# Kernel tuning notes

Hardware: AMD Instinct MI355X
Metric: run time of the kernel (lower is better)

The kernel has to match this reference:

```python
import jax, jax.numpy as jnp
import numpy as np

B, S, H = 2, 2048, 4096
NH, NKV, HD = 32, 8, 128
THETA = 1000000.0
NEG = jnp.finfo(jnp.float32).min


def setup_inputs() -> dict:
    key = jax.random.key(0)
    ks = jax.random.split(key, 9)
    s = 0.02
    return {
        "hidden_states": jax.random.normal(ks[0], (B, S, H), jnp.float32),
        "position_ids": jnp.tile(jnp.arange(S, dtype=jnp.int32)[None, :], (B, 1)),
        "Wq": jax.random.normal(ks[1], (NH * HD, H), jnp.float32) * s,
        "bq": jax.random.normal(ks[2], (NH * HD,), jnp.float32) * s,
        "Wk": jax.random.normal(ks[3], (NKV * HD, H), jnp.float32) * s,
        "bk": jax.random.normal(ks[4], (NKV * HD,), jnp.float32) * s,
        "Wv": jax.random.normal(ks[5], (NKV * HD, H), jnp.float32) * s,
        "bv": jax.random.normal(ks[6], (NKV * HD,), jnp.float32) * s,
        "Wo": jax.random.normal(ks[7], (H, H), jnp.float32) * s,
        "bo": jax.random.normal(ks[8], (H,), jnp.float32) * s,
    }


def _rotate_half_interleaved(x):
    # y[..., ::2] = -x[..., 1::2]; y[..., 1::2] = x[..., ::2]
    x2 = x.reshape(*x.shape[:-1], -1, 2)
    y = jnp.stack([-x2[..., 1], x2[..., 0]], axis=-1)
    return y.reshape(x.shape)


def reference(hidden_states, position_ids, Wq, bq, Wk, bk, Wv, bv, Wo, bo):
    bsz, q_len, _ = hidden_states.shape
    q = (hidden_states @ Wq.T + bq).reshape(bsz, q_len, NH, HD).transpose(0, 2, 1, 3)
    k = (hidden_states @ Wk.T + bk).reshape(bsz, q_len, NKV, HD).transpose(0, 2, 1, 3)
    v = (hidden_states @ Wv.T + bv).reshape(bsz, q_len, NKV, HD).transpose(0, 2, 1, 3)

    # rotary embedding (interleaved / repeat_interleave variant)
    inv_freq = 1.0 / (THETA ** (jnp.arange(0, HD, 2, dtype=jnp.float32) / HD))
    freqs = position_ids.astype(jnp.float32)[:, :, None] * inv_freq[None, None, :]  # [B,S,HD/2]
    emb = jnp.repeat(freqs, 2, axis=-1)  # [B,S,HD]
    cos = jnp.cos(emb)[:, None, :, :]  # [B,1,S,HD]
    sin = jnp.sin(emb)[:, None, :, :]
    q = q * cos + _rotate_half_interleaved(q) * sin
    k = k * cos + _rotate_half_interleaved(k) * sin

    # GQA: repeat KV heads (repeat_interleave on head axis)
    n_rep = NH // NKV
    k = jnp.repeat(k, n_rep, axis=1)
    v = jnp.repeat(v, n_rep, axis=1)

    scores = jnp.einsum("bhqd,bhkd->bhqk", q, k) / np.sqrt(HD).astype(np.float32)
    causal = jnp.tril(jnp.ones((q_len, q_len), dtype=bool))
    scores = jnp.where(causal[None, None, :, :], scores, NEG)
    attn = jax.nn.softmax(scores.astype(jnp.float32), axis=-1).astype(q.dtype)
    out = jnp.einsum("bhqk,bhkd->bhqd", attn, v)
    out = out.transpose(0, 2, 1, 3).reshape(bsz, q_len, H)
    return out @ Wo.T + bo
```

## Files before the change

kernel.cpp:

```cpp
#include <hip/hip_runtime.h>
#include <stdint.h>

typedef __bf16 bf16x8 __attribute__((ext_vector_type(8)));
typedef float f32x4 __attribute__((ext_vector_type(4)));
typedef float f32x16 __attribute__((ext_vector_type(16)));

#define S_LEN 2048
#define NKVH 8
#define HDIM 128
#define MROWS 4096
#define LDQKV 6144
#define SCALE 0.08838834764831845f
#define C_LOG2 0.1275405707067851f
#define THR_RAW 62.7f

__device__ __forceinline__ unsigned short f2bf(float f) {
  unsigned u = __float_as_uint(f);
  u += 0x7FFFu + ((u >> 16) & 1u);
  return (unsigned short)(u >> 16);
}
__device__ __forceinline__ float bf2f(unsigned short h) {
  return __uint_as_float(((unsigned)h) << 16);
}

__device__ __forceinline__ void gload16(const unsigned short* g, unsigned short* l) {
  __builtin_amdgcn_global_load_lds(
      (__attribute__((address_space(1))) void*)(g),
      (__attribute__((address_space(3))) void*)(l), 16, 0, 0);
}

__global__ void cast_f32_bf16(const float4* __restrict__ in, ushort4* __restrict__ out, int n4) {
  int i = blockIdx.x * 256 + threadIdx.x;
  const int stride = gridDim.x * 256;
  for (; i < n4; i += stride) {
    float4 v = in[i];
    ushort4 o;
    o.x = f2bf(v.x); o.y = f2bf(v.y); o.z = f2bf(v.z); o.w = f2bf(v.w);
    out[i] = o;
  }
}

template <int OUTF>
__global__ __launch_bounds__(512, 2)
void gemm256(const unsigned short* __restrict__ A,
             const unsigned short* __restrict__ Bw,
             const float* __restrict__ bias,
             void* __restrict__ C,
             int ldc, int K) {
  __shared__ unsigned short lds[2][4][8192];

  const int t = threadIdx.x;
  const int lane = t & 63;
  const int w = t >> 6;
  const int wr = w >> 2, wc = w & 3;
  const int row16 = lane & 15, kgrp = lane >> 4;
  const int m0 = blockIdx.y * 256, n0 = blockIdx.x * 256;

  const int riu = t >> 3;
  const int col = (((t & 7) ^ (riu & 7)) << 3);
  const int rB0 = (riu & 31) + ((riu >> 5) << 6);
  const unsigned short* pA = A + (size_t)(m0 + riu) * K + col;
  const unsigned short* pB = Bw + (size_t)(n0 + rB0) * K + col;

#define STG(nb_, u_, src_)                                                  \
  {                                                                         \
    gload16((src_), &lds[nb_][u_][t * 8]);                                  \
    gload16((src_) + (size_t)128 * K, &lds[nb_][u_][4096 + t * 8]);         \
  }

  const int sw = row16 & 7;
  const int abase = (wr * 64 + row16) * 64;
  const int bbase = (wc * 32 + row16) * 64;

  f32x4 acc[8][4];
#pragma unroll
  for (int i = 0; i < 8; i++)
#pragma unroll
    for (int j = 0; j < 4; j++) acc[i][j] = (f32x4){0.f, 0.f, 0.f, 0.f};

  bf16x8 afr[4][2], bfr[2][2][2];
  const int NT = K >> 6;

  STG(0, 0, pA);
  STG(0, 1, pB);
  STG(0, 2, pB + (size_t)32 * K);
  STG(0, 3, pA + (size_t)64 * K);

  for (int T = 0; T < NT; ++T) {
    const int cb = T & 1, nb = cb ^ 1;
    const unsigned short* Lc = &lds[cb][0][0];
    const size_t kk = (size_t)(T + 1) << 6;
    const bool st = (T + 1 < NT);

    asm volatile("s_waitcnt vmcnt(4)\n\ts_barrier" ::: "memory");
    if (st) STG(nb, 0, pA + kk);
#pragma unroll
    for (int mi = 0; mi < 4; mi++)
#pragma unroll
      for (int ks = 0; ks < 2; ks++)
        afr[mi][ks] = *(const bf16x8*)(Lc + abase + mi * 1024 + ((((ks << 2) + kgrp) ^ sw) << 3));
#pragma unroll
    for (int nj = 0; nj < 2; nj++)
#pragma unroll
      for (int ks = 0; ks < 2; ks++)
        bfr[0][nj][ks] = *(const bf16x8*)(Lc + 8192 + bbase + nj * 1024 + ((((ks << 2) + kgrp) ^ sw) << 3));
    __builtin_amdgcn_s_setprio(1);
#pragma unroll
    for (int mi = 0; mi < 4; mi++)
#pragma unroll
      for (int nj = 0; nj < 2; nj++)
#pragma unroll
        for (int ks = 0; ks < 2; ks++)
          acc[mi][nj] = __builtin_amdgcn_mfma_f32_16x16x32_bf16(afr[mi][ks], bfr[0][nj][ks], acc[mi][nj], 0, 0, 0);
    __builtin_amdgcn_s_setprio(0);

    if (st) {
      asm volatile("s_waitcnt vmcnt(4)\n\ts_barrier" ::: "memory");
      STG(nb, 1, pB + kk);
    } else {
      asm volatile("s_waitcnt vmcnt(2)\n\ts_barrier" ::: "memory");
    }
#pragma unroll
    for (int nj = 0; nj < 2; nj++)
#pragma unroll
      for (int ks = 0; ks < 2; ks++)
        bfr[1][nj][ks] = *(const bf16x8*)(Lc + 16384 + bbase + nj * 1024 + ((((ks << 2) + kgrp) ^ sw) << 3));
    __builtin_amdgcn_s_setprio(1);
#pragma unroll
    for (int mi = 0; mi < 4; mi++)
#pragma unroll
      for (int nj = 0; nj < 2; nj++)
#pragma unroll
        for (int ks = 0; ks < 2; ks++)
          acc[mi][2 + nj] = __builtin_amdgcn_mfma_f32_16x16x32_bf16(afr[mi][ks], bfr[1][nj][ks], acc[mi][2 + nj], 0, 0, 0);
    __builtin_amdgcn_s_setprio(0);

    if (st) {
      asm volatile("s_waitcnt vmcnt(4)\n\ts_barrier" ::: "memory");
      STG(nb, 2, pB + (size_t)32 * K + kk);
    } else {
      asm volatile("s_waitcnt vmcnt(0)\n\ts_barrier" ::: "memory");
    }
#pragma unroll
    for (int mi = 0; mi < 4; mi++)
#pragma unroll
      for (int ks = 0; ks < 2; ks++)
        afr[mi][ks] = *(const bf16x8*)(Lc + 24576 + abase + mi * 1024 + ((((ks << 2) + kgrp) ^ sw) << 3));
    __builtin_amdgcn_s_setprio(1);
#pragma unroll
    for (int mi = 0; mi < 4; mi++)
#pragma unroll
      for (int nj = 0; nj < 2; nj++)
#pragma unroll
        for (int ks = 0; ks < 2; ks++)
          acc[4 + mi][2 + nj] = __builtin_amdgcn_mfma_f32_16x16x32_bf16(afr[mi][ks], bfr[1][nj][ks], acc[4 + mi][2 + nj], 0, 0, 0);
    __builtin_amdgcn_s_setprio(0);

    if (st) {
      asm volatile("s_waitcnt vmcnt(4)\n\ts_barrier" ::: "memory");
      STG(nb, 3, pA + (size_t)64 * K + kk);
    } else {
      asm volatile("s_barrier" ::: "memory");
    }
    __builtin_amdgcn_s_setprio(1);
#pragma unroll
    for (int mi = 0; mi < 4; mi++)
#pragma unroll
      for (int nj = 0; nj < 2; nj++)
#pragma unroll
        for (int ks = 0; ks < 2; ks++)
          acc[4 + mi][nj] = __builtin_amdgcn_mfma_f32_16x16x32_bf16(afr[mi][ks], bfr[0][nj][ks], acc[4 + mi][nj], 0, 0, 0);
    __builtin_amdgcn_s_setprio(0);
  }
#undef STG

#pragma unroll
  for (int MI = 0; MI < 8; MI++) {
#pragma unroll
    for (int NJ = 0; NJ < 4; NJ++) {
      const int gr = m0 + wr * 128 + MI * 16 + kgrp * 4;
      const int gc = n0 + wc * 64 + NJ * 16 + row16;
      const float bv = bias[gc];
#pragma unroll
      for (int jj = 0; jj < 4; jj++) {
        float v = acc[MI][NJ][jj] + bv;
        if (OUTF) ((float*)C)[(size_t)(gr + jj) * ldc + gc] = v;
        else ((unsigned short*)C)[(size_t)(gr + jj) * ldc + gc] = f2bf(v);
      }
    }
  }
}

template <int OUTF>
__global__ __launch_bounds__(512, 2)
void gemm128(const unsigned short* __restrict__ A,
             const unsigned short* __restrict__ Bw,
             const float* __restrict__ bias,
             void* __restrict__ C,
             int ldc, int K) {
  __shared__ unsigned short lds[3 * 24576];

  const int t = threadIdx.x;
  const int lane = t & 63;
  const int w = t >> 6;
  const int wr = w >> 2, wc = w & 3;
  const int row16 = lane & 15, kgrp = lane >> 4;
  const int m0 = blockIdx.y * 128, n0 = blockIdx.x * 256;

  const int riu = t >> 3;
  const int col = (((t & 7) ^ (riu & 7)) << 3);
  const unsigned short* pA = A + (size_t)(m0 + riu) * K + col;
  const unsigned short* pB = Bw + (size_t)(n0 + riu) * K + col;

#define STG6(bo_, kk_)                                                      \
  {                                                                         \
    gload16(pA + (kk_), &lds[(bo_) + t * 8]);                               \
    gload16(pA + (size_t)64 * K + (kk_), &lds[(bo_) + 4096 + t * 8]);       \
    gload16(pB + (kk_), &lds[(bo_) + 8192 + t * 8]);                        \
    gload16(pB + (size_t)64 * K + (kk_), &lds[(bo_) + 12288 + t * 8]);      \
    gload16(pB + (size_t)128 * K + (kk_), &lds[(bo_) + 16384 + t * 8]);     \
    gload16(pB + (size_t)192 * K + (kk_), &lds[(bo_) + 20480 + t * 8]);     \
  }

  const int sw = row16 & 7;
  const int abase = (wr * 64 + row16) * 64;
  const int bbase = 8192 + (wc * 64 + row16) * 64;

  f32x4 acc[4][4];
#pragma unroll
  for (int i = 0; i < 4; i++)
#pragma unroll
    for (int j = 0; j < 4; j++) acc[i][j] = (f32x4){0.f, 0.f, 0.f, 0.f};

  bf16x8 afr[4][2], bfr[4][2];
  const int NT = K >> 6;

  STG6(0, 0);
  STG6(24576, 64);

  int rbc = 0;
  int rbs = 2;
  for (int T = 0; T < NT; ++T) {
    if (T < NT - 1) { asm volatile("s_waitcnt vmcnt(6)\n\ts_barrier" ::: "memory"); }
    else            { asm volatile("s_waitcnt vmcnt(0)\n\ts_barrier" ::: "memory"); }
    if (T + 2 < NT) STG6(rbs * 24576, (size_t)(T + 2) << 6);
    const unsigned short* Lc = &lds[rbc * 24576];

#pragma unroll
    for (int mi = 0; mi < 4; mi++)
#pragma unroll
      for (int ks = 0; ks < 2; ks++)
        afr[mi][ks] = *(const bf16x8*)(Lc + abase + mi * 1024 + ((((ks << 2) + kgrp) ^ sw) << 3));
#pragma unroll
    for (int nj = 0; nj < 4; nj++)
#pragma unroll
      for (int ks = 0; ks < 2; ks++)
        bfr[nj][ks] = *(const bf16x8*)(Lc + bbase + nj * 1024 + ((((ks << 2) + kgrp) ^ sw) << 3));

    __builtin_amdgcn_s_setprio(1);
#pragma unroll
    for (int mi = 0; mi < 4; mi++)
#pragma unroll
      for (int nj = 0; nj < 4; nj++)
#pragma unroll
        for (int ks = 0; ks < 2; ks++)
          acc[mi][nj] = __builtin_amdgcn_mfma_f32_16x16x32_bf16(afr[mi][ks], bfr[nj][ks], acc[mi][nj], 0, 0, 0);
    __builtin_amdgcn_s_setprio(0);

    rbc++; if (rbc == 3) rbc = 0;
    rbs++; if (rbs == 3) rbs = 0;
  }
#undef STG6

#pragma unroll
  for (int MI = 0; MI < 4; MI++) {
#pragma unroll
    for (int NJ = 0; NJ < 4; NJ++) {
      const int gr = m0 + wr * 64 + MI * 16 + kgrp * 4;
      const int gc = n0 + wc * 64 + NJ * 16 + row16;
      const float bv = bias[gc];
#pragma unroll
      for (int jj = 0; jj < 4; jj++) {
        float v = acc[MI][NJ][jj] + bv;
        if (OUTF) ((float*)C)[(size_t)(gr + jj) * ldc + gc] = v;
        else ((unsigned short*)C)[(size_t)(gr + jj) * ldc + gc] = f2bf(v);
      }
    }
  }
}

__global__ void rope_kernel(unsigned short* __restrict__ X,
                            const int* __restrict__ pos_ids,
                            int ncols, int ld) {
  const int perrow = ncols >> 3;
  int idx = blockIdx.x * 256 + threadIdx.x;
  const int row = idx / perrow;
  const int c0 = (idx - row * perrow) << 3;
  const float pos = (float)pos_ids[row];
  unsigned short* p = X + (size_t)row * ld + c0;
  uint4 v = *(uint4*)p;
  unsigned short* e = (unsigned short*)&v;
  const int p0 = (c0 & 127) >> 1;
#pragma unroll
  for (int q = 0; q < 4; ++q) {
    const float inv = exp2f(-(float)(p0 + q) * (19.931568569324174f / 64.f));
    const float fr = pos * inv;
    float sn, cs;
    __sincosf(fr, &sn, &cs);
    const float xe = bf2f(e[2 * q]);
    const float xo = bf2f(e[2 * q + 1]);
    e[2 * q]     = f2bf(xe * cs - xo * sn);
    e[2 * q + 1] = f2bf(xo * cs + xe * sn);
  }
  *(uint4*)p = v;
}

__global__ void transpose_v(const unsigned short* __restrict__ V, int ldv,
                            unsigned short* __restrict__ Vt) {
  __shared__ unsigned short tile[32][40];
  const int t = threadIdx.x;
  const int n0 = blockIdx.x * 32;
  const int m0 = blockIdx.y * 32;
  const int r = t >> 3;
  const int c = (t & 7) << 2;
  const unsigned short* src = V + (size_t)(m0 + r) * ldv + n0 + c;
  ushort4 d = *(const ushort4*)src;
  tile[r][c] = d.x; tile[r][c + 1] = d.y; tile[r][c + 2] = d.z; tile[r][c + 3] = d.w;
  __syncthreads();
  const int b = m0 >> 11;
  unsigned short* dst = Vt + (size_t)(b * 1024 + n0 + r) * 2048 + (m0 & 2047) + c;
  ushort4 o;
  o.x = tile[c][r]; o.y = tile[c + 1][r]; o.z = tile[c + 2][r]; o.w = tile[c + 3][r];
  *(ushort4*)dst = o;
}

__global__ __launch_bounds__(256, 2)
void attn_kernel3(const unsigned short* __restrict__ QKV,
                  const unsigned short* __restrict__ Vt,
                  unsigned short* __restrict__ O) {
  __shared__ unsigned short sK[64 * 128];
  __shared__ unsigned short sV[128 * 64];

  const int t = threadIdx.x;
  const int lane = t & 63;
  const int w = t >> 6;
  const int l31 = lane & 31;
  const int hi = lane >> 5;
  const int bid = blockIdx.x;
  const int g = bid >> 6, bh = bid & 63;
  const int qt = (g < 4) ? (15 - g) : (g < 8) ? (g - 4) : (g < 12) ? (19 - g) : (g - 8);
  const int b = bh >> 5, h = bh & 31;
  const int kh = h >> 2;
  const int q0 = qt << 7;
  const int qw = q0 + w * 32;
  const int qg = qw + l31;

  const int ntiles = (q0 + 128) >> 6;
  const int myTiles = (qw + 95) >> 6;

  const int krow0 = t >> 4;
  const int kslot = t & 15;
  const int vrow0 = t >> 3;
  const int vslot = t & 7;
  const unsigned short* Kp = QKV + (size_t)(b * S_LEN) * LDQKV + 4096 + kh * HDIM;
  const unsigned short* Vp = Vt + (size_t)(b * 1024 + kh * HDIM) * 2048;
  const int ksw = (kslot ^ (krow0 & 7)) << 3;
  const int vsw = (vslot ^ (vrow0 & 7)) << 3;
  const unsigned short* KpA = Kp + (size_t)krow0 * LDQKV + ksw;
  const unsigned short* VpA = Vp + (size_t)vrow0 * 2048 + vsw;

#define STAGE(kv0m)                                                         \
  {                                                                         \
    _Pragma("unroll")                                                       \
    for (int p = 0; p < 4; p++)                                             \
      gload16(KpA + (size_t)((kv0m) + 16 * p) * LDQKV, &sK[p * 2048 + t * 8]); \
    _Pragma("unroll")                                                       \
    for (int p = 0; p < 4; p++)                                             \
      gload16(VpA + (kv0m) + p * 65536, &sV[p * 2048 + t * 8]);             \
  }

  bf16x8 qf[8];
  {
    const unsigned short* qb = QKV + (size_t)(b * S_LEN + qw + l31) * LDQKV + h * HDIM + hi * 8;
#pragma unroll
    for (int kd = 0; kd < 8; kd++) qf[kd] = *(const bf16x8*)(qb + kd * 16);
  }

  f32x16 o[4];
#pragma unroll
  for (int nt = 0; nt < 4; nt++)
#pragma unroll
    for (int r = 0; r < 16; r++) o[nt][r] = 0.f;
  float m = -1e30f, lsum = 0.f;

  const int rw7 = (l31 & 7) << 4;
  const int kswz = (hi << 4) ^ rw7;
  const int kbase0 = l31 * 128;
  const int vbase = l31 * 64;

  for (int it = 0; it < ntiles; ++it) {
    STAGE(it << 6);
    asm volatile("s_waitcnt vmcnt(0)" ::: "memory");
    __builtin_amdgcn_s_barrier();

    if (it < myTiles) {
      const int kv0 = it << 6;

      f32x16 st[2];
#pragma unroll
      for (int r = 0; r < 16; r++) { st[0][r] = 0.f; st[1][r] = 0.f; }
      __builtin_amdgcn_s_setprio(1);
#pragma unroll
      for (int kd = 0; kd < 8; kd++) {
        bf16x8 k0 = *(const bf16x8*)(sK + kbase0 + (((kd << 5) ^ kswz) >> 1));
        bf16x8 k1 = *(const bf16x8*)(sK + 4096 + kbase0 + (((kd << 5) ^ kswz) >> 1));
        st[0] = __builtin_amdgcn_mfma_f32_32x32x16_bf16(k0, qf[kd], st[0], 0, 0, 0);
        st[1] = __builtin_amdgcn_mfma_f32_32x32x16_bf16(k1, qf[kd], st[1], 0, 0, 0);
      }
      __builtin_amdgcn_s_setprio(0);

      if (it == myTiles - 1) {
#pragma unroll
        for (int s2 = 0; s2 < 2; s2++)
#pragma unroll
          for (int r = 0; r < 16; r++) {
            const int kvg = kv0 + s2 * 32 + (r & 3) + 8 * (r >> 2) + 4 * hi;
            if (kvg > qg) st[s2][r] = -1e30f;
          }
      }

      float mx[8];
#pragma unroll
      for (int r = 0; r < 8; r++)
        mx[r] = fmaxf(fmaxf(st[0][r], st[0][r + 8]), fmaxf(st[1][r], st[1][r + 8]));
#pragma unroll
      for (int d = 4; d >= 1; d >>= 1)
#pragma unroll
        for (int r = 0; r < d; r++) mx[r] = fmaxf(mx[r], mx[r + d]);
      float tmax = fmaxf(mx[0], __shfl_xor(mx[0], 32));

      if (!__all(tmax <= m + THR_RAW)) {
        const float mnew = fmaxf(m, tmax);
        const float corr = exp2f((m - mnew) * C_LOG2);
        lsum *= corr;
#pragma unroll
        for (int r = 0; r < 16; r++) {
          const int src = (r & 3) + 8 * (r >> 2) + 4 * hi;
          const float cr = __shfl(corr, src);
#pragma unroll
          for (int nt = 0; nt < 4; nt++) o[nt][r] *= cr;
        }
        m = mnew;
      }
      const float mC = m * C_LOG2;

#pragma unroll
      for (int s2 = 0; s2 < 2; s2++)
#pragma unroll
        for (int r = 0; r < 16; r++) st[s2][r] = exp2f(fmaf(st[s2][r], C_LOG2, -mC));
      float sm[8];
#pragma unroll
      for (int r = 0; r < 8; r++)
        sm[r] = (st[0][r] + st[0][r + 8]) + (st[1][r] + st[1][r + 8]);
#pragma unroll
      for (int d = 4; d >= 1; d >>= 1)
#pragma unroll
        for (int r = 0; r < d; r++) sm[r] += sm[r + d];
      float tsum = sm[0] + __shfl_xor(sm[0], 32);
      lsum += tsum;

      bf16x8 pa[4];
#pragma unroll
      for (int s2 = 0; s2 < 2; s2++) {
        unsigned pw[8];
#pragma unroll
        for (int i = 0; i < 8; i++)
          asm("v_cvt_pk_bf16_f32 %0, %1, %2" : "=v"(pw[i]) : "v"(st[s2][2 * i]), "v"(st[s2][2 * i + 1]));
        const unsigned x0 = (unsigned)__shfl_xor((int)pw[0], 32);
        const unsigned x1 = (unsigned)__shfl_xor((int)pw[1], 32);
        const unsigned x2 = (unsigned)__shfl_xor((int)pw[2], 32);
        const unsigned x3 = (unsigned)__shfl_xor((int)pw[3], 32);
        const unsigned x4 = (unsigned)__shfl_xor((int)pw[4], 32);
        const unsigned x5 = (unsigned)__shfl_xor((int)pw[5], 32);
        const unsigned x6 = (unsigned)__shfl_xor((int)pw[6], 32);
        const unsigned x7 = (unsigned)__shfl_xor((int)pw[7], 32);
        union { unsigned u[4]; bf16x8 v; } u0, u1;
        u0.u[0] = hi ? x2 : pw[0];
        u0.u[1] = hi ? x3 : pw[1];
        u0.u[2] = hi ? pw[2] : x0;
        u0.u[3] = hi ? pw[3] : x1;
        u1.u[0] = hi ? x6 : pw[4];
        u1.u[1] = hi ? x7 : pw[5];
        u1.u[2] = hi ? pw[6] : x4;
        u1.u[3] = hi ? pw[7] : x5;
        pa[2 * s2] = u0.v; pa[2 * s2 + 1] = u1.v;
      }

      __builtin_amdgcn_s_setprio(1);
#pragma unroll
      for (int nt = 0; nt < 4; nt++) {
        const unsigned short* vr = sV + vbase + nt * 2048;
#pragma unroll
        for (int ks = 0; ks < 4; ks++) {
          bf16x8 vb = *(const bf16x8*)(vr + (((ks << 5) ^ kswz) >> 1));
          o[nt] = __builtin_amdgcn_mfma_f32_32x32x16_bf16(pa[ks], vb, o[nt], 0, 0, 0);
        }
      }
      __builtin_amdgcn_s_setprio(0);
    }

    __builtin_amdgcn_s_barrier();
  }

  const float linv = 1.0f / lsum;
#pragma unroll
  for (int r = 0; r < 16; r++) {
    const int qr = (r & 3) + 8 * (r >> 2) + 4 * hi;
    const float lr = __shfl(linv, qr);
    unsigned short* orow = O + (size_t)(b * S_LEN + qw + qr) * 4096 + h * HDIM + l31;
#pragma unroll
    for (int nt = 0; nt < 4; nt++) orow[nt * 32] = f2bf(o[nt][r] * lr);
  }
#undef STAGE
}

extern "C" void kernel_launch(void* const* d_in, const int* in_sizes, int n_in,
                              void* d_out, int out_size, void* d_ws, size_t ws_size,
                              hipStream_t stream) {
  const float* hs = (const float*)d_in[0];
  const int*  pos = (const int*)d_in[1];
  const float* Wq = (const float*)d_in[2];
  const float* bq = (const float*)d_in[3];
  const float* Wk = (const float*)d_in[4];
  const float* bk = (const float*)d_in[5];
  const float* Wv = (const float*)d_in[6];
  const float* bv = (const float*)d_in[7];
  const float* Wo = (const float*)d_in[8];
  const float* bo = (const float*)d_in[9];
  float* out = (float*)d_out;

  char* ws = (char*)d_ws;
  unsigned short* hbf  = (unsigned short*)(ws);
  unsigned short* Wbuf = (unsigned short*)(ws + 33554432);
  unsigned short* QKV  = (unsigned short*)(ws + 83886080);
  unsigned short* Vtb  = (unsigned short*)(ws + 134217728);
  float*          biasb= (float*)(ws + 142606336);

  cast_f32_bf16<<<2048, 256, 0, stream>>>((const float4*)hs, (ushort4*)hbf, 4194304);
  cast_f32_bf16<<<2048, 256, 0, stream>>>((const float4*)Wq, (ushort4*)Wbuf, 4194304);
  cast_f32_bf16<<<1024, 256, 0, stream>>>((const float4*)Wk, (ushort4*)(Wbuf + 16777216), 1048576);
  cast_f32_bf16<<<1024, 256, 0, stream>>>((const float4*)Wv, (ushort4*)(Wbuf + 20971520), 1048576);
  hipMemcpyAsync(biasb, bq, 4096 * 4, hipMemcpyDeviceToDevice, stream);
  hipMemcpyAsync(biasb + 4096, bk, 1024 * 4, hipMemcpyDeviceToDevice, stream);
  hipMemcpyAsync(biasb + 5120, bv, 1024 * 4, hipMemcpyDeviceToDevice, stream);

  gemm256<0><<<dim3(16, 16), 512, 0, stream>>>(hbf, Wbuf, biasb, QKV, LDQKV, 4096);
  gemm128<0><<<dim3(8, 32), 512, 0, stream>>>(hbf, Wbuf + 16777216, biasb + 4096, QKV + 4096, LDQKV, 4096);

  cast_f32_bf16<<<2048, 256, 0, stream>>>((const float4*)Wo, (ushort4*)Wbuf, 4194304);

  rope_kernel<<<8192, 256, 0, stream>>>(QKV, pos, 4096, LDQKV);
  rope_kernel<<<2048, 256, 0, stream>>>(QKV + 4096, pos, 1024, LDQKV);

  transpose_v<<<dim3(32, 128), 256, 0, stream>>>(QKV + 5120, LDQKV, Vtb);

  attn_kernel3<<<dim3(1024), 256, 0, stream>>>(QKV, Vtb, hbf);

  gemm256<1><<<dim3(16, 16), 512, 0, stream>>>(hbf, Wbuf, bo, out, 4096, 4096);
}
```

Baseline: 519.1 us.

## Double-buffer K/V shared tiles in attention and simplify q-tile ordering

Doubles the shared-memory K and V buffers so the next KV tile is prefetched with async global-to-LDS loads while the current tile is computed. The wait drops to vmcnt(8) so only the previous tile's loads must finish, hiding load latency. It also changes the block-to-query-tile ordering to a simpler heavy-first then light schedule. Shared memory use doubles to 64KB per block, which may reduce occupancy below the two blocks per CU requested by launch bounds.

```diff
diff --git a/kernel.cpp b/kernel.cpp
--- a/kernel.cpp
+++ b/kernel.cpp
@@ -338,8 +338,8 @@
 void attn_kernel3(const unsigned short* __restrict__ QKV,
                   const unsigned short* __restrict__ Vt,
                   unsigned short* __restrict__ O) {
-  __shared__ unsigned short sK[64 * 128];
-  __shared__ unsigned short sV[128 * 64];
+  __shared__ unsigned short sK[2 * 64 * 128];
+  __shared__ unsigned short sV[2 * 128 * 64];
 
   const int t = threadIdx.x;
   const int lane = t & 63;
@@ -348,7 +348,7 @@
   const int hi = lane >> 5;
   const int bid = blockIdx.x;
   const int g = bid >> 6, bh = bid & 63;
-  const int qt = (g < 4) ? (15 - g) : (g < 8) ? (g - 4) : (g < 12) ? (19 - g) : (g - 8);
+  const int qt = (g < 8) ? (15 - g) : (g - 8);
   const int b = bh >> 5, h = bh & 31;
   const int kh = h >> 2;
   const int q0 = qt << 7;
@@ -369,14 +369,15 @@
   const unsigned short* KpA = Kp + (size_t)krow0 * LDQKV + ksw;
   const unsigned short* VpA = Vp + (size_t)vrow0 * 2048 + vsw;
 
-#define STAGE(kv0m)                                                         \
-  {                                                                         \
-    _Pragma("unroll")                                                       \
-    for (int p = 0; p < 4; p++)                                             \
-      gload16(KpA + (size_t)((kv0m) + 16 * p) * LDQKV, &sK[p * 2048 + t * 8]); \
-    _Pragma("unroll")                                                       \
-    for (int p = 0; p < 4; p++)                                             \
-      gload16(VpA + (kv0m) + p * 65536, &sV[p * 2048 + t * 8]);             \
+#define STAGE(bufi, kv0m)                                                      \
+  {                                                                            \
+    _Pragma("unroll")                                                          \
+    for (int p = 0; p < 4; p++)                                                \
+      gload16(KpA + (size_t)((kv0m) + 16 * p) * LDQKV,                         \
+              &sK[(bufi) * 8192 + p * 2048 + t * 8]);                          \
+    _Pragma("unroll")                                                          \
+    for (int p = 0; p < 4; p++)                                                \
+      gload16(VpA + (kv0m) + p * 65536, &sV[(bufi) * 8192 + p * 2048 + t * 8]); \
   }
 
   bf16x8 qf[8];
@@ -398,12 +399,20 @@
   const int kbase0 = l31 * 128;
   const int vbase = l31 * 64;
 
+  STAGE(0, 0);
+  int buf = 0;
   for (int it = 0; it < ntiles; ++it) {
-    STAGE(it << 6);
-    asm volatile("s_waitcnt vmcnt(0)" ::: "memory");
+    if (it + 1 < ntiles) {
+      STAGE(buf ^ 1, (it + 1) << 6);
+      asm volatile("s_waitcnt vmcnt(8)" ::: "memory");
+    } else {
+      asm volatile("s_waitcnt vmcnt(0)" ::: "memory");
+    }
     __builtin_amdgcn_s_barrier();
 
     if (it < myTiles) {
+      const unsigned short* sKc = sK + buf * 8192;
+      const unsigned short* sVc = sV + buf * 8192;
       const int kv0 = it << 6;
 
       f32x16 st[2];
@@ -412,8 +421,8 @@
       __builtin_amdgcn_s_setprio(1);
 #pragma unroll
       for (int kd = 0; kd < 8; kd++) {
-        bf16x8 k0 = *(const bf16x8*)(sK + kbase0 + (((kd << 5) ^ kswz) >> 1));
-        bf16x8 k1 = *(const bf16x8*)(sK + 4096 + kbase0 + (((kd << 5) ^ kswz) >> 1));
+        bf16x8 k0 = *(const bf16x8*)(sKc + kbase0 + (((kd << 5) ^ kswz) >> 1));
+        bf16x8 k1 = *(const bf16x8*)(sKc + 4096 + kbase0 + (((kd << 5) ^ kswz) >> 1));
         st[0] = __builtin_amdgcn_mfma_f32_32x32x16_bf16(k0, qf[kd], st[0], 0, 0, 0);
         st[1] = __builtin_amdgcn_mfma_f32_32x32x16_bf16(k1, qf[kd], st[1], 0, 0, 0);
       }
@@ -499,7 +508,7 @@
       __builtin_amdgcn_s_setprio(1);
 #pragma unroll
       for (int nt = 0; nt < 4; nt++) {
-        const unsigned short* vr = sV + vbase + nt * 2048;
+        const unsigned short* vr = sVc + vbase + nt * 2048;
 #pragma unroll
         for (int ks = 0; ks < 4; ks++) {
           bf16x8 vb = *(const bf16x8*)(vr + (((ks << 5) ^ kswz) >> 1));
@@ -510,6 +519,7 @@
     }
 
     __builtin_amdgcn_s_barrier();
+    buf ^= 1;
   }
 
   const float linv = 1.0f / lsum;
```

After: 520.8 us. No clear change (+0.3%).
